# Performance work log

Hardware: AMD Instinct MI355X
Metric: run time of the kernel (lower is better)

The kernel has to match this reference:

```python
import jax, jax.numpy as jnp
import numpy as np

N, DF, DR, H, K = 4096, 128, 64, 1024, 10


def _init_linear(key, fan_in, fan_out):
    kw, kb = jax.random.split(key)
    bound = 1.0 / np.sqrt(fan_in)
    W = jax.random.uniform(kw, (fan_in, fan_out), jnp.float32, -bound, bound)
    b = jax.random.uniform(kb, (fan_out,), jnp.float32, -bound, bound)
    return W, b


def setup_inputs() -> dict:
    key = jax.random.key(0)
    ks = jax.random.split(key, 8)
    condition = jax.random.normal(ks[0], (N, DF), jnp.float32)
    tensor = jax.random.normal(ks[1], (N, DR), jnp.float32)
    Win, b_in = _init_linear(ks[2], DF + DR, H)
    W1, b1 = _init_linear(ks[3], H, H)
    W2, b2 = _init_linear(ks[4], H, H)
    W3, b3 = _init_linear(ks[5], H, H)
    Wout, b_out = _init_linear(ks[6], H, DR)
    return {"condition": condition, "tensor": tensor,
            "Win": Win, "b_in": b_in, "W1": W1, "b1": b1,
            "W2": W2, "b2": b2, "W3": W3, "b3": b3,
            "Wout": Wout, "b_out": b_out}


def _mlp(x, Win, b_in, W1, b1, W2, b2, W3, b3, Wout, b_out):
    # FFNN: input layer + 3 hidden layers with Softplus, linear output -> DR
    h = jax.nn.softplus(x @ Win + b_in)
    h = jax.nn.softplus(h @ W1 + b1)
    h = jax.nn.softplus(h @ W2 + b2)
    h = jax.nn.softplus(h @ W3 + b3)
    return h @ Wout + b_out


def reference(condition, tensor, Win, b_in, W1, b1, W2, b2, W3, b3, Wout, b_out):
    # torch.cdist(condition, condition), p=2 -> [N, N]
    sq = jnp.sum(condition * condition, axis=-1)
    d2 = sq[:, None] + sq[None, :] - 2.0 * (condition @ condition.T)
    dist = jnp.sqrt(jnp.maximum(d2, 0.0))
    # torch.topk(dist, 10, dim=1, largest=False) -> k nearest neighbor indices
    _, neighbor_idx = jax.lax.top_k(-dist, K)  # [N, K]
    # gather neighbor groups
    cond_g = condition[neighbor_idx]  # [N, K, DF]
    tens_g = tensor[neighbor_idx]     # [N, K, DR]
    # MongeMapNetwork.pushforward: tensor - MLP(concat(condition, tensor))
    x = jnp.concatenate([cond_g, tens_g], axis=-1)  # [N, K, DF+DR]
    pushed = tens_g - _mlp(x, Win, b_in, W1, b1, W2, b2, W3, b3, Wout, b_out)
    return pushed  # [N, K, DR]
```

## Files before the change

kernel.cpp:

```cpp
#include <hip/hip_runtime.h>
#include <stdint.h>

typedef unsigned short u16;
typedef unsigned int   u32;
typedef unsigned long long u64;
typedef short v8bf __attribute__((ext_vector_type(8)));
typedef float v4f  __attribute__((ext_vector_type(4)));

#define NPTS 4096
#define DF   128
#define DR   64
#define HID  1024
#define KNN  10
#define MROWS (NPTS*KNN)
#define DIN  192

#define AS1 __attribute__((address_space(1)))
#define AS3 __attribute__((address_space(3)))

__device__ __forceinline__ float bf2f(u16 b){ return __uint_as_float(((unsigned)b)<<16); }
__device__ __forceinline__ u16 f2bf(float f){
  unsigned u = __float_as_uint(f);
  unsigned r = 0x7fffu + ((u>>16)&1u);
  return (u16)((u + r)>>16);
}
__device__ __forceinline__ float softplus_f(float x){
  return x>15.f ? x : __logf(1.f + __expf(x));
}
__device__ __forceinline__ float rdv(const void* p, long j, int fl){
  return fl ? bf2f(((const u16*)p)[j]) : ((const float*)p)[j];
}
__device__ __forceinline__ void gl2lds16(const u16* g, u16* l){
  __builtin_amdgcn_global_load_lds((const AS1 unsigned int*)g, (AS3 unsigned int*)l, 16, 0, 0);
}

__global__ void detect_k(const u16* __restrict__ c, int* __restrict__ flag){
  __shared__ int cnt[256];
  int t = threadIdx.x, n = 0;
  for(int i=t; i<8192; i+=256){
    u16 v = c[2*i];
    int e = (v>>7)&0xff;
    n += (e>=96 && e<=158);
  }
  cnt[t] = n; __syncthreads();
  for(int s=128; s>0; s>>=1){ if(t<s) cnt[t]+=cnt[t+s]; __syncthreads(); }
  if(t==0) *flag = (cnt[0] > 4915) ? 1 : 0;
}

__global__ void prep_k(const void* cond, const void* tens,
    const void* Wi, const void* W1, const void* W2, const void* W3, const void* Wo,
    const void* bi, const void* b1, const void* b2, const void* b3, const void* bo,
    float* __restrict__ condF, float* __restrict__ tensF, float* __restrict__ biasF,
    u16* Oi, u16* O1, u16* O2, u16* O3, u16* Oo,
    float* __restrict__ sq, u16* __restrict__ X, const int* __restrict__ flag){
  __shared__ u16 tile[32][33];
  const int fl = *flag;
  const int bid = blockIdx.x, tid = threadIdx.x;
  if(bid < 3089){
    int i = bid*256 + tid;
    if(i < 524288){ condF[i] = rdv(cond, i, fl); }
    else if(i < 786432){ tensF[i-524288] = rdv(tens, i-524288, fl); }
    else{
      int j = i - 786432;
      if(j < 1024)      biasF[j] = rdv(bi, j, fl);
      else if(j < 2048) biasF[j] = rdv(b1, j-1024, fl);
      else if(j < 3072) biasF[j] = rdv(b2, j-2048, fl);
      else if(j < 4096) biasF[j] = rdv(b3, j-3072, fl);
      else if(j < 4160) biasF[j] = rdv(bo, j-4096, fl);
    }
  } else if(bid < 6417){
    int b = bid - 3089;
    const void* in; u16* out; int R, C, bx, by;
    if(b < 192)      {              in=Wi; out=Oi; R=192;  C=1024; bx=b&31; by=b>>5; }
    else if(b < 1216){ b -= 192;    in=W1; out=O1; R=1024; C=1024; bx=b&31; by=b>>5; }
    else if(b < 2240){ b -= 1216;   in=W2; out=O2; R=1024; C=1024; bx=b&31; by=b>>5; }
    else if(b < 3264){ b -= 2240;   in=W3; out=O3; R=1024; C=1024; bx=b&31; by=b>>5; }
    else             { b -= 3264;   in=Wo; out=Oo; R=1024; C=64;   bx=b&1;  by=b>>1; }
    int gx = bx*32, gy = by*32;
    int tx = tid&31, ty = tid>>5;
    #pragma unroll
    for(int r=ty; r<32; r+=8){
      size_t idx = (size_t)(gy+r)*C + gx + tx;
      tile[r][tx] = fl ? ((const u16*)in)[idx] : f2bf(((const float*)in)[idx]);
    }
    __syncthreads();
    #pragma unroll
    for(int r=ty; r<32; r+=8) out[(size_t)(gx+r)*R + gy + tx] = tile[tx][r];
  } else if(bid < 7441){
    int b = bid - 6417;
    int row = b*4 + (tid>>6), lane = tid&63;
    float a = rdv(cond, (long)row*DF + lane, fl);
    float c2 = rdv(cond, (long)row*DF + lane + 64, fl);
    double s = (double)a*a + (double)c2*c2;
    #pragma unroll
    for(int off=32; off>0; off>>=1) s += __shfl_down(s, off, 64);
    if(lane==0) sq[row] = (float)s;
  } else {
    int c = (bid-7441)*256 + tid;
    int j = c/48;
    int off = (c - j*48)*4;
    ushort4 o;
    if(off < DF){
      o.x = f2bf(rdv(cond, (long)j*DF + off + 0, fl));
      o.y = f2bf(rdv(cond, (long)j*DF + off + 1, fl));
      o.z = f2bf(rdv(cond, (long)j*DF + off + 2, fl));
      o.w = f2bf(rdv(cond, (long)j*DF + off + 3, fl));
    }else{
      int t2 = off - DF;
      o.x = f2bf(rdv(tens, (long)j*DR + t2 + 0, fl));
      o.y = f2bf(rdv(tens, (long)j*DR + t2 + 1, fl));
      o.z = f2bf(rdv(tens, (long)j*DR + t2 + 2, fl));
      o.w = f2bf(rdv(tens, (long)j*DR + t2 + 3, fl));
    }
    *(ushort4*)&X[(size_t)j*DIN + off] = o;
  }
}

__global__ __launch_bounds__(256) void gram_dist_k(const u16* __restrict__ condB,
    const float* __restrict__ condF, const float* __restrict__ sq,
    float* __restrict__ dist, const int* __restrict__ flag){
  __shared__ u16 Ahi[128*40], Alo[128*40], Bhi[128*40], Blo[128*40];
  const int fl = *flag;
  const int bm = blockIdx.x*128, bn = blockIdx.y*128;
  const int tid = threadIdx.x, lane = tid&63, wave = tid>>6;
  const int wm = (wave&1)*64, wn = (wave>>1)*64;
  v4f acc[4][4] = {};
  for(int kb=0; kb<DF; kb+=32){
    if(fl){
      #pragma unroll
      for(int t=0;t<2;t++){
        int c2 = tid + t*256;
        int r = c2>>2, col = (c2&3)*8;
        *(uint4*)&Ahi[r*40+col] = *(const uint4*)&condB[(size_t)(bm+r)*DF + kb + col];
        *(uint4*)&Bhi[r*40+col] = *(const uint4*)&condB[(size_t)(bn+r)*DF + kb + col];
      }
    }else{
      #pragma unroll
      for(int t=0;t<4;t++){
        int ch = tid + t*256;
        int r = ch>>3, c = (ch&7)*4;
        float4 av = *(const float4*)&condF[(size_t)(bm+r)*DF + kb + c];
        float4 bv = *(const float4*)&condF[(size_t)(bn+r)*DF + kb + c];
        ushort4 ah, bh, al, bl;
        ah.x=f2bf(av.x); ah.y=f2bf(av.y); ah.z=f2bf(av.z); ah.w=f2bf(av.w);
        bh.x=f2bf(bv.x); bh.y=f2bf(bv.y); bh.z=f2bf(bv.z); bh.w=f2bf(bv.w);
        al.x=f2bf(av.x-bf2f(ah.x)); al.y=f2bf(av.y-bf2f(ah.y));
        al.z=f2bf(av.z-bf2f(ah.z)); al.w=f2bf(av.w-bf2f(ah.w));
        bl.x=f2bf(bv.x-bf2f(bh.x)); bl.y=f2bf(bv.y-bf2f(bh.y));
        bl.z=f2bf(bv.z-bf2f(bh.z)); bl.w=f2bf(bv.w-bf2f(bh.w));
        *(ushort4*)&Ahi[r*40+c] = ah; *(ushort4*)&Bhi[r*40+c] = bh;
        *(ushort4*)&Alo[r*40+c] = al; *(ushort4*)&Blo[r*40+c] = bl;
      }
    }
    __syncthreads();
    const int m16 = lane&15, q = lane>>4;
    v8bf ahf[4], bhf[4];
    #pragma unroll
    for(int x=0;x<4;x++){
      ahf[x] = *(const v8bf*)&Ahi[(wm + x*16 + m16)*40 + q*8];
      bhf[x] = *(const v8bf*)&Bhi[(wn + x*16 + m16)*40 + q*8];
    }
    if(!fl){
      v8bf alf[4], blf[4];
      #pragma unroll
      for(int x=0;x<4;x++){
        alf[x] = *(const v8bf*)&Alo[(wm + x*16 + m16)*40 + q*8];
        blf[x] = *(const v8bf*)&Blo[(wn + x*16 + m16)*40 + q*8];
      }
      #pragma unroll
      for(int mi=0;mi<4;mi++)
        #pragma unroll
        for(int ni=0;ni<4;ni++){
          acc[mi][ni] = __builtin_amdgcn_mfma_f32_16x16x32_bf16(alf[mi], bhf[ni], acc[mi][ni], 0,0,0);
          acc[mi][ni] = __builtin_amdgcn_mfma_f32_16x16x32_bf16(ahf[mi], blf[ni], acc[mi][ni], 0,0,0);
        }
    }
    #pragma unroll
    for(int mi=0;mi<4;mi++)
      #pragma unroll
      for(int ni=0;ni<4;ni++)
        acc[mi][ni] = __builtin_amdgcn_mfma_f32_16x16x32_bf16(ahf[mi], bhf[ni], acc[mi][ni], 0,0,0);
    __syncthreads();
  }
  const int col16 = lane&15, rowq = lane>>4;
  #pragma unroll
  for(int mi=0;mi<4;mi++){
    #pragma unroll
    for(int ni=0;ni<4;ni++){
      int cj = bn + wn + ni*16 + col16;
      float sqj = sq[cj];
      #pragma unroll
      for(int r=0;r<4;r++){
        int ri = bm + wm + mi*16 + rowq*4 + r;
        float d2 = (sq[ri] + sqj) - 2.0f*acc[mi][ni][r];
        dist[(size_t)ri*NPTS + cj] = fmaxf(d2, 0.f);
      }
    }
  }
}

__global__ __launch_bounds__(256) void knn_k(const float* __restrict__ dist,
    const float* __restrict__ condF, int* __restrict__ nidx){
  const int tid = threadIdx.x, lane = tid&63, wv = tid>>6;
  const int row = blockIdx.x*4 + wv;
  __shared__ float af[4][DF];
  __shared__ int   scnt[4];
  __shared__ int   cand[4][64];
  __shared__ u64   keys[4][64];
  af[wv][lane]    = condF[(size_t)row*DF + lane];
  af[wv][lane+64] = condF[(size_t)row*DF + lane + 64];
  if(lane==0) scnt[wv] = 0;
  const float4* drow4 = (const float4*)(dist + (size_t)row*NPTS);
  float4 vals[16];
  #pragma unroll
  for(int k=0;k<16;k++) vals[k] = drow4[lane + k*64];
  float mx = 0.f;
  #pragma unroll
  for(int k=0;k<16;k++)
    mx = fmaxf(mx, fmaxf(fmaxf(vals[k].x,vals[k].y), fmaxf(vals[k].z,vals[k].w)));
  #pragma unroll
  for(int off=32; off>0; off>>=1) mx = fmaxf(mx, __shfl_down(mx, off, 64));
  mx = __shfl(mx, 0, 64);
  float hi = mx*1.000001f + 1e-6f, lo = 0.f;
  for(int it=0; it<18; ++it){
    float mid = 0.5f*(lo+hi);
    int c = 0;
    #pragma unroll
    for(int k=0;k<16;k++)
      c += (vals[k].x<mid) + (vals[k].y<mid) + (vals[k].z<mid) + (vals[k].w<mid);
    #pragma unroll
    for(int off=32; off>0; off>>=1) c += __shfl_down(c, off, 64);
    c = __shfl(c, 0, 64);
    if(c >= 16){ hi = mid; if(c <= 48) break; }
    else lo = mid;
  }
  const float t = hi;
  #pragma unroll
  for(int k=0;k<16;k++){
    float v[4] = {vals[k].x, vals[k].y, vals[k].z, vals[k].w};
    #pragma unroll
    for(int e=0;e<4;e++){
      if(v[e] < t){
        int s = atomicAdd(&scnt[wv], 1);
        if(s < 64) cand[wv][s] = (lane + k*64)*4 + e;
      }
    }
  }
  int cnt = scnt[wv]; if(cnt > 64) cnt = 64;
  u64 mykey = ~0ULL; int myj = -1;
  if(lane < cnt){
    int j = cand[wv][lane];
    const float4* bp4 = (const float4*)(condF + (size_t)j*DF);
    const float* ap = af[wv];
    double s = 0.0;
    #pragma unroll
    for(int v4i=0; v4i<32; v4i++){
      float4 bv = bp4[v4i];
      double d0 = (double)ap[v4i*4+0]-(double)bv.x;
      double d1 = (double)ap[v4i*4+1]-(double)bv.y;
      double d2 = (double)ap[v4i*4+2]-(double)bv.z;
      double d3 = (double)ap[v4i*4+3]-(double)bv.w;
      s += d0*d0 + d1*d1 + d2*d2 + d3*d3;
    }
    u64 bits = (u64)__double_as_longlong(s);
    mykey = (bits & ~0xFFFULL) | (u32)j;
    myj = j;
  }
  keys[wv][lane] = mykey;
  if(lane < cnt){
    int rank = 0;
    for(int c2=0;c2<cnt;c2++) rank += (keys[wv][c2] < mykey);
    if(rank < KNN) nidx[row*KNN + rank] = myj;
  }
}

template<int ACT>
__global__ __launch_bounds__(256,2) void gemm_bt_k(const u16* __restrict__ A,
    const u16* __restrict__ Bt, const float* __restrict__ bias, u16* __restrict__ C,
    int Nc, int Kc){
  __shared__ u16 As[128*32];
  __shared__ u16 Bs[64*32];
  const int bid = blockIdx.x;
  const int xcd = bid&7, slot = bid>>3;
  const int bm = (xcd*4 + (slot>>4)) * 128;
  const int bn = (slot&15) * 64;
  const int tid = threadIdx.x, lane = tid&63, wave = tid>>6;
  const int wm = (wave&1)*64, wn = (wave>>1)*32;
  int c0 = wave*128 + lane, c1 = c0 + 64;
  int r0 = c0>>2, q0 = c0&3, r1 = c1>>2, q1 = c1&3;
  int cb = wave*64 + lane, rb = cb>>2, qb = cb&3;
  const u16* pA0 = A  + (size_t)(bm+r0)*Kc + q0*8;
  const u16* pA1 = A  + (size_t)(bm+r1)*Kc + q1*8;
  const u16* pB  = Bt + (size_t)(bn+rb)*Kc + qb*8;
  u16* lA0 = &As[(wave*128      )*8];
  u16* lA1 = &As[(wave*128 + 64 )*8];
  u16* lB  = &Bs[(wave*64       )*8];
  const int m16 = lane&15, q = lane>>4;
  v4f acc[4][2] = {};
  for(int kb=0; kb<Kc; kb+=32){
    gl2lds16(pA0 + kb, lA0);
    gl2lds16(pA1 + kb, lA1);
    gl2lds16(pB  + kb, lB);
    __syncthreads();
    v8bf a[4], b[2];
    #pragma unroll
    for(int x=0;x<4;x++) a[x] = *(const v8bf*)&As[(wm + x*16 + m16)*32 + q*8];
    #pragma unroll
    for(int x=0;x<2;x++) b[x] = *(const v8bf*)&Bs[(wn + x*16 + m16)*32 + q*8];
    #pragma unroll
    for(int mi=0;mi<4;mi++)
      #pragma unroll
      for(int ni=0;ni<2;ni++)
        acc[mi][ni] = __builtin_amdgcn_mfma_f32_16x16x32_bf16(a[mi], b[ni], acc[mi][ni], 0,0,0);
    __syncthreads();
  }
  const int col16 = lane&15, rowq = lane>>4;
  #pragma unroll
  for(int mi=0;mi<4;mi++){
    #pragma unroll
    for(int ni=0;ni<2;ni++){
      int cn = bn + wn + ni*16 + col16;
      float bi = bias[cn];
      #pragma unroll
      for(int r=0;r<4;r++){
        int rw = bm + wm + mi*16 + rowq*4 + r;
        float v = acc[mi][ni][r] + bi;
        if(ACT) v = softplus_f(v);
        C[(size_t)rw*Nc + cn] = f2bf(v);
      }
    }
  }
}

__global__ __launch_bounds__(256,2) void gemm_out_k(const u16* __restrict__ A,
    const u16* __restrict__ Bt, const float* __restrict__ bias,
    const float* __restrict__ tensF, float* __restrict__ P){
  __shared__ u16 As[128*32];
  __shared__ u16 Bs[64*32];
  const int bm = blockIdx.x*128;
  const int tid = threadIdx.x, lane = tid&63, wave = tid>>6;
  const int wm = wave*32;
  int c0 = wave*128 + lane, c1 = c0 + 64;
  int ra0 = c0>>2, qa0 = c0&3, ra1 = c1>>2, qa1 = c1&3;
  int cb = wave*64 + lane;
  int rb = cb>>2, qb = cb&3;
  const u16* pA0 = A  + (size_t)(bm+ra0)*HID + qa0*8;
  const u16* pA1 = A  + (size_t)(bm+ra1)*HID + qa1*8;
  const u16* pB  = Bt + (size_t)rb*HID + qb*8;
  u16* lA0 = &As[(wave*128     )*8];
  u16* lA1 = &As[(wave*128 + 64)*8];
  u16* lB  = &Bs[(wave*64      )*8];
  const int m16 = lane&15, q = lane>>4;
  v4f acc[2][4] = {};
  for(int kb=0; kb<HID; kb+=32){
    gl2lds16(pA0 + kb, lA0);
    gl2lds16(pA1 + kb, lA1);
    gl2lds16(pB  + kb, lB);
    __syncthreads();
    v8bf a[2], b[4];
    a[0] = *(const v8bf*)&As[(wm + m16)*32 + q*8];
    a[1] = *(const v8bf*)&As[(wm + 16 + m16)*32 + q*8];
    #pragma unroll
    for(int x=0;x<4;x++) b[x] = *(const v8bf*)&Bs[(x*16 + m16)*32 + q*8];
    #pragma unroll
    for(int mi=0;mi<2;mi++)
      #pragma unroll
      for(int ni=0;ni<4;ni++)
        acc[mi][ni] = __builtin_amdgcn_mfma_f32_16x16x32_bf16(a[mi], b[ni], acc[mi][ni], 0,0,0);
    __syncthreads();
  }
  const int col16 = lane&15, rowq = lane>>4;
  #pragma unroll
  for(int mi=0;mi<2;mi++){
    #pragma unroll
    for(int ni=0;ni<4;ni++){
      int cn = ni*16 + col16;
      float bi = bias[cn];
      #pragma unroll
      for(int r=0;r<4;r++){
        int rw = bm + wm + mi*16 + rowq*4 + r;
        P[(size_t)rw*DR + cn] = tensF[(size_t)rw*DR + cn] - (acc[mi][ni][r] + bi);
      }
    }
  }
}

__global__ void gather_k(const float* __restrict__ P, const int* __restrict__ nidx,
                         void* __restrict__ outv, const int* __restrict__ flag){
  const int fl = *flag;
  int e = blockIdx.x*256 + threadIdx.x;
  int m = e>>4;
  int c = (e&15)*4;
  int j = nidx[m] & (NPTS-1);
  float4 v = *(const float4*)&P[(size_t)j*DR + c];
  if(fl){
    ushort4 o; o.x=f2bf(v.x); o.y=f2bf(v.y); o.z=f2bf(v.z); o.w=f2bf(v.w);
    *(ushort4*)&((u16*)outv)[(size_t)m*DR + c] = o;
  }else{
    *(float4*)&((float*)outv)[(size_t)m*DR + c] = v;
  }
}

constexpr size_t OFF_FLAG  = 0;
constexpr size_t OFF_SQ    = 256;
constexpr size_t OFF_NIDX  = OFF_SQ    + 16384;
constexpr size_t OFF_BIAS  = OFF_NIDX  + 163840;
constexpr size_t OFF_CONDF = OFF_BIAS  + 16640;
constexpr size_t OFF_TENSF = OFF_CONDF + 2097152;
constexpr size_t OFF_WTIN  = OFF_TENSF + 1048576;
constexpr size_t OFF_WT1   = OFF_WTIN  + 393216;
constexpr size_t OFF_WT2   = OFF_WT1   + 2097152;
constexpr size_t OFF_WT3   = OFF_WT2   + 2097152;
constexpr size_t OFF_WTO   = OFF_WT3   + 2097152;
constexpr size_t OFF_RA    = OFF_WTO   + 131072;
constexpr size_t OFF_RB    = OFF_RA    + 83886080;
constexpr size_t OFF_P     = OFF_RB    + 83886080;

extern "C" void kernel_launch(void* const* d_in, const int* in_sizes, int n_in,
                              void* d_out, int out_size, void* d_ws, size_t ws_size,
                              hipStream_t stream){
  char* ws = (char*)d_ws;
  int*   flag  = (int*)  (ws + OFF_FLAG);
  float* sqv   = (float*)(ws + OFF_SQ);
  int*   nidx  = (int*)  (ws + OFF_NIDX);
  float* biasF = (float*)(ws + OFF_BIAS);
  float* condF = (float*)(ws + OFF_CONDF);
  float* tensF = (float*)(ws + OFF_TENSF);
  u16*   Wt_in = (u16*)  (ws + OFF_WTIN);
  u16*   Wt1   = (u16*)  (ws + OFF_WT1);
  u16*   Wt2   = (u16*)  (ws + OFF_WT2);
  u16*   Wt3   = (u16*)  (ws + OFF_WT3);
  u16*   Wt_o  = (u16*)  (ws + OFF_WTO);
  float* dist  = (float*)(ws + OFF_RA);
  u16*   A0    = (u16*)  (ws + OFF_RA);
  u16*   X     = (u16*)  (ws + OFF_RB);
  u16*   A1    = (u16*)  (ws + OFF_RB);
  float* P     = (float*)(ws + OFF_P);

  detect_k <<<1, 256, 0, stream>>>((const u16*)d_in[0], flag);
  prep_k   <<<8209, 256, 0, stream>>>(d_in[0], d_in[1],
                d_in[2], d_in[4], d_in[6], d_in[8], d_in[10],
                d_in[3], d_in[5], d_in[7], d_in[9], d_in[11],
                condF, tensF, biasF, Wt_in, Wt1, Wt2, Wt3, Wt_o, sqv, X, flag);
  gram_dist_k<<<dim3(32,32), 256, 0, stream>>>((const u16*)d_in[0], condF, sqv, dist, flag);
  knn_k      <<<1024, 256, 0, stream>>>(dist, condF, nidx);
  gemm_bt_k<1><<<512, 256, 0, stream>>>(X,  Wt_in, biasF,      A0, HID, DIN);
  gemm_bt_k<1><<<512, 256, 0, stream>>>(A0, Wt1,   biasF+1024, A1, HID, HID);
  gemm_bt_k<1><<<512, 256, 0, stream>>>(A1, Wt2,   biasF+2048, A0, HID, HID);
  gemm_bt_k<1><<<512, 256, 0, stream>>>(A0, Wt3,   biasF+3072, A1, HID, HID);
  gemm_out_k  <<<32, 256, 0, stream>>>(A1, Wt_o, biasF+4096, tensF, P);
  gather_k    <<<2560, 256, 0, stream>>>(P, nidx, d_out, flag);
}
```

Baseline: 238.2 us.

## Co-schedule independent distance/KNN work with MLP GEMMs and split-K output layer

Merges the Gram-distance kernel with the first MLP GEMM, and the KNN selection with the next two hidden GEMMs, as heterogeneous blocks inside one launch. Independent work can then fill idle CUs and fewer launches are needed. The output GEMM is split four ways over K to raise its grid from 32 to 128 blocks, with the partial sums, bias and tensor subtraction moved into the gather. This needs separate workspace buffers for dist and activations, raises shared memory per block in the fused kernels, and adds four partial-buffer reads in the gather.

```diff
diff --git a/kernel.cpp b/kernel.cpp
--- a/kernel.cpp
+++ b/kernel.cpp
@@ -12,7 +12,6 @@
 #define DR   64
 #define HID  1024
 #define KNN  10
-#define MROWS (NPTS*KNN)
 #define DIN  192
 
 #define AS1 __attribute__((address_space(1)))
@@ -116,171 +115,9 @@
   }
 }
 
-__global__ __launch_bounds__(256) void gram_dist_k(const u16* __restrict__ condB,
-    const float* __restrict__ condF, const float* __restrict__ sq,
-    float* __restrict__ dist, const int* __restrict__ flag){
-  __shared__ u16 Ahi[128*40], Alo[128*40], Bhi[128*40], Blo[128*40];
-  const int fl = *flag;
-  const int bm = blockIdx.x*128, bn = blockIdx.y*128;
-  const int tid = threadIdx.x, lane = tid&63, wave = tid>>6;
-  const int wm = (wave&1)*64, wn = (wave>>1)*64;
-  v4f acc[4][4] = {};
-  for(int kb=0; kb<DF; kb+=32){
-    if(fl){
-      #pragma unroll
-      for(int t=0;t<2;t++){
-        int c2 = tid + t*256;
-        int r = c2>>2, col = (c2&3)*8;
-        *(uint4*)&Ahi[r*40+col] = *(const uint4*)&condB[(size_t)(bm+r)*DF + kb + col];
-        *(uint4*)&Bhi[r*40+col] = *(const uint4*)&condB[(size_t)(bn+r)*DF + kb + col];
-      }
-    }else{
-      #pragma unroll
-      for(int t=0;t<4;t++){
-        int ch = tid + t*256;
-        int r = ch>>3, c = (ch&7)*4;
-        float4 av = *(const float4*)&condF[(size_t)(bm+r)*DF + kb + c];
-        float4 bv = *(const float4*)&condF[(size_t)(bn+r)*DF + kb + c];
-        ushort4 ah, bh, al, bl;
-        ah.x=f2bf(av.x); ah.y=f2bf(av.y); ah.z=f2bf(av.z); ah.w=f2bf(av.w);
-        bh.x=f2bf(bv.x); bh.y=f2bf(bv.y); bh.z=f2bf(bv.z); bh.w=f2bf(bv.w);
-        al.x=f2bf(av.x-bf2f(ah.x)); al.y=f2bf(av.y-bf2f(ah.y));
-        al.z=f2bf(av.z-bf2f(ah.z)); al.w=f2bf(av.w-bf2f(ah.w));
-        bl.x=f2bf(bv.x-bf2f(bh.x)); bl.y=f2bf(bv.y-bf2f(bh.y));
-        bl.z=f2bf(bv.z-bf2f(bh.z)); bl.w=f2bf(bv.w-bf2f(bh.w));
-        *(ushort4*)&Ahi[r*40+c] = ah; *(ushort4*)&Bhi[r*40+c] = bh;
-        *(ushort4*)&Alo[r*40+c] = al; *(ushort4*)&Blo[r*40+c] = bl;
-      }
-    }
-    __syncthreads();
-    const int m16 = lane&15, q = lane>>4;
-    v8bf ahf[4], bhf[4];
-    #pragma unroll
-    for(int x=0;x<4;x++){
-      ahf[x] = *(const v8bf*)&Ahi[(wm + x*16 + m16)*40 + q*8];
-      bhf[x] = *(const v8bf*)&Bhi[(wn + x*16 + m16)*40 + q*8];
-    }
-    if(!fl){
-      v8bf alf[4], blf[4];
-      #pragma unroll
-      for(int x=0;x<4;x++){
-        alf[x] = *(const v8bf*)&Alo[(wm + x*16 + m16)*40 + q*8];
-        blf[x] = *(const v8bf*)&Blo[(wn + x*16 + m16)*40 + q*8];
-      }
-      #pragma unroll
-      for(int mi=0;mi<4;mi++)
-        #pragma unroll
-        for(int ni=0;ni<4;ni++){
-          acc[mi][ni] = __builtin_amdgcn_mfma_f32_16x16x32_bf16(alf[mi], bhf[ni], acc[mi][ni], 0,0,0);
-          acc[mi][ni] = __builtin_amdgcn_mfma_f32_16x16x32_bf16(ahf[mi], blf[ni], acc[mi][ni], 0,0,0);
-        }
-    }
-    #pragma unroll
-    for(int mi=0;mi<4;mi++)
-      #pragma unroll
-      for(int ni=0;ni<4;ni++)
-        acc[mi][ni] = __builtin_amdgcn_mfma_f32_16x16x32_bf16(ahf[mi], bhf[ni], acc[mi][ni], 0,0,0);
-    __syncthreads();
-  }
-  const int col16 = lane&15, rowq = lane>>4;
-  #pragma unroll
-  for(int mi=0;mi<4;mi++){
-    #pragma unroll
-    for(int ni=0;ni<4;ni++){
-      int cj = bn + wn + ni*16 + col16;
-      float sqj = sq[cj];
-      #pragma unroll
-      for(int r=0;r<4;r++){
-        int ri = bm + wm + mi*16 + rowq*4 + r;
-        float d2 = (sq[ri] + sqj) - 2.0f*acc[mi][ni][r];
-        dist[(size_t)ri*NPTS + cj] = fmaxf(d2, 0.f);
-      }
-    }
-  }
-}
-
-__global__ __launch_bounds__(256) void knn_k(const float* __restrict__ dist,
-    const float* __restrict__ condF, int* __restrict__ nidx){
-  const int tid = threadIdx.x, lane = tid&63, wv = tid>>6;
-  const int row = blockIdx.x*4 + wv;
-  __shared__ float af[4][DF];
-  __shared__ int   scnt[4];
-  __shared__ int   cand[4][64];
-  __shared__ u64   keys[4][64];
-  af[wv][lane]    = condF[(size_t)row*DF + lane];
-  af[wv][lane+64] = condF[(size_t)row*DF + lane + 64];
-  if(lane==0) scnt[wv] = 0;
-  const float4* drow4 = (const float4*)(dist + (size_t)row*NPTS);
-  float4 vals[16];
-  #pragma unroll
-  for(int k=0;k<16;k++) vals[k] = drow4[lane + k*64];
-  float mx = 0.f;
-  #pragma unroll
-  for(int k=0;k<16;k++)
-    mx = fmaxf(mx, fmaxf(fmaxf(vals[k].x,vals[k].y), fmaxf(vals[k].z,vals[k].w)));
-  #pragma unroll
-  for(int off=32; off>0; off>>=1) mx = fmaxf(mx, __shfl_down(mx, off, 64));
-  mx = __shfl(mx, 0, 64);
-  float hi = mx*1.000001f + 1e-6f, lo = 0.f;
-  for(int it=0; it<18; ++it){
-    float mid = 0.5f*(lo+hi);
-    int c = 0;
-    #pragma unroll
-    for(int k=0;k<16;k++)
-      c += (vals[k].x<mid) + (vals[k].y<mid) + (vals[k].z<mid) + (vals[k].w<mid);
-    #pragma unroll
-    for(int off=32; off>0; off>>=1) c += __shfl_down(c, off, 64);
-    c = __shfl(c, 0, 64);
-    if(c >= 16){ hi = mid; if(c <= 48) break; }
-    else lo = mid;
-  }
-  const float t = hi;
-  #pragma unroll
-  for(int k=0;k<16;k++){
-    float v[4] = {vals[k].x, vals[k].y, vals[k].z, vals[k].w};
-    #pragma unroll
-    for(int e=0;e<4;e++){
-      if(v[e] < t){
-        int s = atomicAdd(&scnt[wv], 1);
-        if(s < 64) cand[wv][s] = (lane + k*64)*4 + e;
-      }
-    }
-  }
-  int cnt = scnt[wv]; if(cnt > 64) cnt = 64;
-  u64 mykey = ~0ULL; int myj = -1;
-  if(lane < cnt){
-    int j = cand[wv][lane];
-    const float4* bp4 = (const float4*)(condF + (size_t)j*DF);
-    const float* ap = af[wv];
-    double s = 0.0;
-    #pragma unroll
-    for(int v4i=0; v4i<32; v4i++){
-      float4 bv = bp4[v4i];
-      double d0 = (double)ap[v4i*4+0]-(double)bv.x;
-      double d1 = (double)ap[v4i*4+1]-(double)bv.y;
-      double d2 = (double)ap[v4i*4+2]-(double)bv.z;
-      double d3 = (double)ap[v4i*4+3]-(double)bv.w;
-      s += d0*d0 + d1*d1 + d2*d2 + d3*d3;
-    }
-    u64 bits = (u64)__double_as_longlong(s);
-    mykey = (bits & ~0xFFFULL) | (u32)j;
-    myj = j;
-  }
-  keys[wv][lane] = mykey;
-  if(lane < cnt){
-    int rank = 0;
-    for(int c2=0;c2<cnt;c2++) rank += (keys[wv][c2] < mykey);
-    if(rank < KNN) nidx[row*KNN + rank] = myj;
-  }
-}
-
-template<int ACT>
-__global__ __launch_bounds__(256,2) void gemm_bt_k(const u16* __restrict__ A,
+__device__ __forceinline__ void gemm_bt_body(const u16* __restrict__ A,
     const u16* __restrict__ Bt, const float* __restrict__ bias, u16* __restrict__ C,
-    int Nc, int Kc){
-  __shared__ u16 As[128*32];
-  __shared__ u16 Bs[64*32];
-  const int bid = blockIdx.x;
+    int Nc, int Kc, int bid, u16* As, u16* Bs){
   const int xcd = bid&7, slot = bid>>3;
   const int bm = (xcd*4 + (slot>>4)) * 128;
   const int bn = (slot&15) * 64;
@@ -324,20 +161,212 @@
       #pragma unroll
       for(int r=0;r<4;r++){
         int rw = bm + wm + mi*16 + rowq*4 + r;
-        float v = acc[mi][ni][r] + bi;
-        if(ACT) v = softplus_f(v);
+        float v = softplus_f(acc[mi][ni][r] + bi);
         C[(size_t)rw*Nc + cn] = f2bf(v);
       }
     }
   }
 }
 
+__device__ __forceinline__ void knn_body(const float* __restrict__ dist,
+    const float* __restrict__ condF, int* __restrict__ nidx, int row,
+    float* __restrict__ af, int* __restrict__ scnt,
+    int* __restrict__ cand, u64* __restrict__ keys){
+  const int lane = threadIdx.x&63;
+  af[lane]    = condF[(size_t)row*DF + lane];
+  af[lane+64] = condF[(size_t)row*DF + lane + 64];
+  if(lane==0) *scnt = 0;
+  const float4* drow4 = (const float4*)(dist + (size_t)row*NPTS);
+  float4 vals[16];
+  #pragma unroll
+  for(int k=0;k<16;k++) vals[k] = drow4[lane + k*64];
+  float mx = 0.f;
+  #pragma unroll
+  for(int k=0;k<16;k++)
+    mx = fmaxf(mx, fmaxf(fmaxf(vals[k].x,vals[k].y), fmaxf(vals[k].z,vals[k].w)));
+  #pragma unroll
+  for(int off=32; off>0; off>>=1) mx = fmaxf(mx, __shfl_down(mx, off, 64));
+  mx = __shfl(mx, 0, 64);
+  float hi = mx*1.000001f + 1e-6f, lo = 0.f;
+  for(int it=0; it<18; ++it){
+    float mid = 0.5f*(lo+hi);
+    int c = 0;
+    #pragma unroll
+    for(int k=0;k<16;k++)
+      c += (vals[k].x<mid) + (vals[k].y<mid) + (vals[k].z<mid) + (vals[k].w<mid);
+    #pragma unroll
+    for(int off=32; off>0; off>>=1) c += __shfl_down(c, off, 64);
+    c = __shfl(c, 0, 64);
+    if(c >= 16){ hi = mid; if(c <= 48) break; }
+    else lo = mid;
+  }
+  const float t = hi;
+  #pragma unroll
+  for(int k=0;k<16;k++){
+    float v[4] = {vals[k].x, vals[k].y, vals[k].z, vals[k].w};
+    #pragma unroll
+    for(int e=0;e<4;e++){
+      if(v[e] < t){
+        int s = atomicAdd(scnt, 1);
+        if(s < 64) cand[s] = (lane + k*64)*4 + e;
+      }
+    }
+  }
+  int cnt = *scnt; if(cnt > 64) cnt = 64;
+  u64 mykey = ~0ULL; int myj = -1;
+  if(lane < cnt){
+    int j = cand[lane];
+    const float4* bp4 = (const float4*)(condF + (size_t)j*DF);
+    double s = 0.0;
+    #pragma unroll
+    for(int v4i=0; v4i<32; v4i++){
+      float4 bv = bp4[v4i];
+      double d0 = (double)af[v4i*4+0]-(double)bv.x;
+      double d1 = (double)af[v4i*4+1]-(double)bv.y;
+      double d2 = (double)af[v4i*4+2]-(double)bv.z;
+      double d3 = (double)af[v4i*4+3]-(double)bv.w;
+      s += d0*d0 + d1*d1 + d2*d2 + d3*d3;
+    }
+    u64 bits = (u64)__double_as_longlong(s);
+    mykey = (bits & ~0xFFFULL) | (u32)j;
+    myj = j;
+  }
+  keys[lane] = mykey;
+  if(lane < cnt){
+    int rank = 0;
+    for(int c2=0;c2<cnt;c2++) rank += (keys[c2] < mykey);
+    if(rank < KNN) nidx[row*KNN + rank] = myj;
+  }
+}
+
+__global__ __launch_bounds__(256,2) void gram_g1_k(const u16* __restrict__ condB,
+    const float* __restrict__ condF, const float* __restrict__ sq,
+    float* __restrict__ dist, const int* __restrict__ flag,
+    const u16* __restrict__ X, const u16* __restrict__ Wt_in,
+    const float* __restrict__ biasF, u16* __restrict__ A0){
+  __shared__ __align__(16) u16 smem[20480];
+  const int bid = blockIdx.x;
+  if(bid < 512){
+    gemm_bt_body(X, Wt_in, biasF, A0, HID, DIN, bid, smem, smem+4096);
+    return;
+  }
+  const int gb = bid - 512;
+  u16* Ahi = smem;
+  u16* Alo = smem + 5120;
+  u16* Bhi = smem + 10240;
+  u16* Blo = smem + 15360;
+  const int fl = *flag;
+  const int bm = (gb&31)*128, bn = (gb>>5)*128;
+  const int tid = threadIdx.x, lane = tid&63, wave = tid>>6;
+  const int wm = (wave&1)*64, wn = (wave>>1)*64;
+  v4f acc[4][4] = {};
+  for(int kb=0; kb<DF; kb+=32){
+    if(fl){
+      #pragma unroll
+      for(int t=0;t<2;t++){
+        int c2 = tid + t*256;
+        int r = c2>>2, col = (c2&3)*8;
+        *(uint4*)&Ahi[r*40+col] = *(const uint4*)&condB[(size_t)(bm+r)*DF + kb + col];
+        *(uint4*)&Bhi[r*40+col] = *(const uint4*)&condB[(size_t)(bn+r)*DF + kb + col];
+      }
+    }else{
+      #pragma unroll
+      for(int t=0;t<4;t++){
+        int ch = tid + t*256;
+        int r = ch>>3, c = (ch&7)*4;
+        float4 av = *(const float4*)&condF[(size_t)(bm+r)*DF + kb + c];
+        float4 bv = *(const float4*)&condF[(size_t)(bn+r)*DF + kb + c];
+        ushort4 ah, bh, al, bl;
+        ah.x=f2bf(av.x); ah.y=f2bf(av.y); ah.z=f2bf(av.z); ah.w=f2bf(av.w);
+        bh.x=f2bf(bv.x); bh.y=f2bf(bv.y); bh.z=f2bf(bv.z); bh.w=f2bf(bv.w);
+        al.x=f2bf(av.x-bf2f(ah.x)); al.y=f2bf(av.y-bf2f(ah.y));
+        al.z=f2bf(av.z-bf2f(ah.z)); al.w=f2bf(av.w-bf2f(ah.w));
+        bl.x=f2bf(bv.x-bf2f(bh.x)); bl.y=f2bf(bv.y-bf2f(bh.y));
+        bl.z=f2bf(bv.z-bf2f(bh.z)); bl.w=f2bf(bv.w-bf2f(bh.w));
+        *(ushort4*)&Ahi[r*40+c] = ah; *(ushort4*)&Bhi[r*40+c] = bh;
+        *(ushort4*)&Alo[r*40+c] = al; *(ushort4*)&Blo[r*40+c] = bl;
+      }
+    }
+    __syncthreads();
+    const int m16 = lane&15, q = lane>>4;
+    v8bf ahf[4], bhf[4];
+    #pragma unroll
+    for(int x=0;x<4;x++){
+      ahf[x] = *(const v8bf*)&Ahi[(wm + x*16 + m16)*40 + q*8];
+      bhf[x] = *(const v8bf*)&Bhi[(wn + x*16 + m16)*40 + q*8];
+    }
+    if(!fl){
+      v8bf alf[4], blf[4];
+      #pragma unroll
+      for(int x=0;x<4;x++){
+        alf[x] = *(const v8bf*)&Alo[(wm + x*16 + m16)*40 + q*8];
+        blf[x] = *(const v8bf*)&Blo[(wn + x*16 + m16)*40 + q*8];
+      }
+      #pragma unroll
+      for(int mi=0;mi<4;mi++)
+        #pragma unroll
+        for(int ni=0;ni<4;ni++){
+          acc[mi][ni] = __builtin_amdgcn_mfma_f32_16x16x32_bf16(alf[mi], bhf[ni], acc[mi][ni], 0,0,0);
+          acc[mi][ni] = __builtin_amdgcn_mfma_f32_16x16x32_bf16(ahf[mi], blf[ni], acc[mi][ni], 0,0,0);
+        }
+    }
+    #pragma unroll
+    for(int mi=0;mi<4;mi++)
+      #pragma unroll
+      for(int ni=0;ni<4;ni++)
+        acc[mi][ni] = __builtin_amdgcn_mfma_f32_16x16x32_bf16(ahf[mi], bhf[ni], acc[mi][ni], 0,0,0);
+    __syncthreads();
+  }
+  const int col16 = lane&15, rowq = lane>>4;
+  #pragma unroll
+  for(int mi=0;mi<4;mi++){
+    #pragma unroll
+    for(int ni=0;ni<4;ni++){
+      int cj = bn + wn + ni*16 + col16;
+      float sqj = sq[cj];
+      #pragma unroll
+      for(int r=0;r<4;r++){
+        int ri = bm + wm + mi*16 + rowq*4 + r;
+        float d2 = (sq[ri] + sqj) - 2.0f*acc[mi][ni][r];
+        dist[(size_t)ri*NPTS + cj] = fmaxf(d2, 0.f);
+      }
+    }
+  }
+}
+
+__global__ __launch_bounds__(256,2) void gemm_knn_k(const u16* __restrict__ A,
+    const u16* __restrict__ Bt, const float* __restrict__ bias, u16* __restrict__ C,
+    const float* __restrict__ dist, const float* __restrict__ condF,
+    int* __restrict__ nidx, int rowoff){
+  __shared__ __align__(16) u16 gsm[6144];
+  __shared__ float af[4][DF];
+  __shared__ int   scnt[4];
+  __shared__ int   cand[4][64];
+  __shared__ u64   keys[4][64];
+  const int bid = blockIdx.x;
+  if(bid < 512){
+    gemm_bt_body(A, Bt, bias, C, HID, HID, bid, gsm, gsm+4096);
+  } else {
+    const int wv = threadIdx.x>>6;
+    const int row = rowoff + (bid-512)*4 + wv;
+    knn_body(dist, condF, nidx, row, af[wv], &scnt[wv], cand[wv], keys[wv]);
+  }
+}
+
+__global__ __launch_bounds__(256,2) void gemm_bt_k(const u16* __restrict__ A,
+    const u16* __restrict__ Bt, const float* __restrict__ bias, u16* __restrict__ C){
+  __shared__ __align__(16) u16 As[128*32];
+  __shared__ __align__(16) u16 Bs[64*32];
+  gemm_bt_body(A, Bt, bias, C, HID, HID, blockIdx.x, As, Bs);
+}
+
 __global__ __launch_bounds__(256,2) void gemm_out_k(const u16* __restrict__ A,
-    const u16* __restrict__ Bt, const float* __restrict__ bias,
-    const float* __restrict__ tensF, float* __restrict__ P){
-  __shared__ u16 As[128*32];
-  __shared__ u16 Bs[64*32];
-  const int bm = blockIdx.x*128;
+    const u16* __restrict__ Bt, float* __restrict__ Pp){
+  __shared__ __align__(16) u16 As[128*32];
+  __shared__ __align__(16) u16 Bs[64*32];
+  const int bm = (blockIdx.x>>2)*128;
+  const int k0 = (blockIdx.x&3)*256;
+  float* P = Pp + (size_t)(blockIdx.x&3)*262144;
   const int tid = threadIdx.x, lane = tid&63, wave = tid>>6;
   const int wm = wave*32;
   int c0 = wave*128 + lane, c1 = c0 + 64;
@@ -352,7 +381,7 @@
   u16* lB  = &Bs[(wave*64      )*8];
   const int m16 = lane&15, q = lane>>4;
   v4f acc[2][4] = {};
-  for(int kb=0; kb<HID; kb+=32){
+  for(int kb=k0; kb<k0+256; kb+=32){
     gl2lds16(pA0 + kb, lA0);
     gl2lds16(pA1 + kb, lA1);
     gl2lds16(pB  + kb, lB);
@@ -375,24 +404,35 @@
     #pragma unroll
     for(int ni=0;ni<4;ni++){
       int cn = ni*16 + col16;
-      float bi = bias[cn];
       #pragma unroll
       for(int r=0;r<4;r++){
         int rw = bm + wm + mi*16 + rowq*4 + r;
-        P[(size_t)rw*DR + cn] = tensF[(size_t)rw*DR + cn] - (acc[mi][ni][r] + bi);
-      }
-    }
-  }
-}
-
-__global__ void gather_k(const float* __restrict__ P, const int* __restrict__ nidx,
+        P[(size_t)rw*DR + cn] = acc[mi][ni][r];
+      }
+    }
+  }
+}
+
+__global__ void gather_k(const float* __restrict__ Pp, const float* __restrict__ tensF,
+                         const float* __restrict__ biasF, const int* __restrict__ nidx,
                          void* __restrict__ outv, const int* __restrict__ flag){
   const int fl = *flag;
   int e = blockIdx.x*256 + threadIdx.x;
   int m = e>>4;
   int c = (e&15)*4;
   int j = nidx[m] & (NPTS-1);
-  float4 v = *(const float4*)&P[(size_t)j*DR + c];
+  size_t rc = (size_t)j*DR + c;
+  float4 t  = *(const float4*)&tensF[rc];
+  float4 b  = *(const float4*)&biasF[4096 + c];
+  float4 p0 = *(const float4*)&Pp[rc];
+  float4 p1 = *(const float4*)&Pp[262144 + rc];
+  float4 p2 = *(const float4*)&Pp[524288 + rc];
+  float4 p3 = *(const float4*)&Pp[786432 + rc];
+  float4 v;
+  v.x = t.x - (b.x + ((p0.x+p1.x)+(p2.x+p3.x)));
+  v.y = t.y - (b.y + ((p0.y+p1.y)+(p2.y+p3.y)));
+  v.z = t.z - (b.z + ((p0.z+p1.z)+(p2.z+p3.z)));
+  v.w = t.w - (b.w + ((p0.w+p1.w)+(p2.w+p3.w)));
   if(fl){
     ushort4 o; o.x=f2bf(v.x); o.y=f2bf(v.y); o.z=f2bf(v.z); o.w=f2bf(v.w);
     *(ushort4*)&((u16*)outv)[(size_t)m*DR + c] = o;
@@ -412,9 +452,11 @@
 constexpr size_t OFF_WT2   = OFF_WT1   + 2097152;
 constexpr size_t OFF_WT3   = OFF_WT2   + 2097152;
 constexpr size_t OFF_WTO   = OFF_WT3   + 2097152;
-constexpr size_t OFF_RA    = OFF_WTO   + 131072;
-constexpr size_t OFF_RB    = OFF_RA    + 83886080;
-constexpr size_t OFF_P     = OFF_RB    + 83886080;
+constexpr size_t OFF_DIST  = OFF_WTO   + 131072;
+constexpr size_t OFF_X     = OFF_DIST  + 67108864;
+constexpr size_t OFF_A0    = OFF_X     + 1572864;
+constexpr size_t OFF_A1    = OFF_A0    + 8388608;
+constexpr size_t OFF_P     = OFF_A1    + 8388608;
 
 extern "C" void kernel_launch(void* const* d_in, const int* in_sizes, int n_in,
                               void* d_out, int out_size, void* d_ws, size_t ws_size,
@@ -431,23 +473,22 @@
   u16*   Wt2   = (u16*)  (ws + OFF_WT2);
   u16*   Wt3   = (u16*)  (ws + OFF_WT3);
   u16*   Wt_o  = (u16*)  (ws + OFF_WTO);
-  float* dist  = (float*)(ws + OFF_RA);
-  u16*   A0    = (u16*)  (ws + OFF_RA);
-  u16*   X     = (u16*)  (ws + OFF_RB);
-  u16*   A1    = (u16*)  (ws + OFF_RB);
-  float* P     = (float*)(ws + OFF_P);
+  float* dist  = (float*)(ws + OFF_DIST);
+  u16*   X     = (u16*)  (ws + OFF_X);
+  u16*   A0    = (u16*)  (ws + OFF_A0);
+  u16*   A1    = (u16*)  (ws + OFF_A1);
+  float* Pp    = (float*)(ws + OFF_P);
 
   detect_k <<<1, 256, 0, stream>>>((const u16*)d_in[0], flag);
   prep_k   <<<8209, 256, 0, stream>>>(d_in[0], d_in[1],
                 d_in[2], d_in[4], d_in[6], d_in[8], d_in[10],
                 d_in[3], d_in[5], d_in[7], d_in[9], d_in[11],
                 condF, tensF, biasF, Wt_in, Wt1, Wt2, Wt3, Wt_o, sqv, X, flag);
-  gram_dist_k<<<dim3(32,32), 256, 0, stream>>>((const u16*)d_in[0], condF, sqv, dist, flag);
-  knn_k      <<<1024, 256, 0, stream>>>(dist, condF, nidx);
-  gemm_bt_k<1><<<512, 256, 0, stream>>>(X,  Wt_in, biasF,      A0, HID, DIN);
-  gemm_bt_k<1><<<512, 256, 0, stream>>>(A0, Wt1,   biasF+1024, A1, HID, HID);
-  gemm_bt_k<1><<<512, 256, 0, stream>>>(A1, Wt2,   biasF+2048, A0, HID, HID);
-  gemm_bt_k<1><<<512, 256, 0, stream>>>(A0, Wt3,   biasF+3072, A1, HID, HID);
-  gemm_out_k  <<<32, 256, 0, stream>>>(A1, Wt_o, biasF+4096, tensF, P);
-  gather_k    <<<2560, 256, 0, stream>>>(P, nidx, d_out, flag);
-}
+  gram_g1_k<<<1536, 256, 0, stream>>>((const u16*)d_in[0], condF, sqv, dist, flag,
+                                      X, Wt_in, biasF, A0);
+  gemm_knn_k<<<1024, 256, 0, stream>>>(A0, Wt1, biasF+1024, A1, dist, condF, nidx, 0);
+  gemm_knn_k<<<1024, 256, 0, stream>>>(A1, Wt2, biasF+2048, A0, dist, condF, nidx, 2048);
+  gemm_bt_k  <<<512, 256, 0, stream>>>(A0, Wt3, biasF+3072, A1);
+  gemm_out_k <<<128, 256, 0, stream>>>(A1, Wt_o, Pp);
+  gather_k   <<<2560, 256, 0, stream>>>(Pp, tensF, biasF, nidx, d_out, flag);
+}
```

New measurement: 214.6 us. -9.9%, faster.
